# Optimization experiments

Measured on AMD Instinct MI355X. Metric: run time of the kernel, lower is better.

## Reference

```python
import jax, jax.numpy as jnp
import numpy as np

B, H, W, D = 16, 14, 14, 512   # map_dim D == attention_dim A (required by broadcast add)
L, HID, A = 32, 512, 512


def setup_inputs() -> dict:
    key = jax.random.key(0)
    ks = jax.random.split(key, 8)
    s = 0.02
    return {
        "maps": jax.random.normal(ks[0], (B, H, W, D), jnp.float32),
        "hiddens": jax.random.normal(ks[1], (B, L, HID), jnp.float32),
        "W_hidden": jax.random.normal(ks[2], (A, HID), jnp.float32) * s,
        "b_hidden": jnp.zeros((A,), jnp.float32),
        "W_rect": jax.random.normal(ks[3], (1, A), jnp.float32) * s,
        "b_rect": jnp.zeros((1,), jnp.float32),
        "W_co": jax.random.normal(ks[4], (HID, D), jnp.float32) * s,
        "b_co": jnp.zeros((HID,), jnp.float32),
    }


def reference(maps, hiddens, W_hidden, b_hidden, W_rect, b_rect, W_co, b_co):
    b, h, w, d = maps.shape
    fmaps = maps.reshape(b, h * w, d)                       # (B, P, D)
    hlin = hiddens @ W_hidden.T + b_hidden                  # (B, L, A)
    # additive co-attention score: ReLU(fmaps + hlin) -> linear to scalar
    rect = jax.nn.relu(fmaps[:, None, :, :] + hlin[:, :, None, :])  # (B, L, P, A)
    scores = jnp.einsum('blpa,a->blp', rect, W_rect[0]) + b_rect[0]  # (B, L, P)
    attn = jax.nn.softmax(scores, axis=2)                   # softmax over pixels P
    ctx = jnp.einsum('blp,bpd->bld', attn, fmaps)           # (B, L, D)
    co_att = (ctx @ W_co.T + b_co) * hiddens                # (B, L, HID)
    return co_att, attn
```

## Files before the change

### kernel.cpp

```cpp
#include <hip/hip_runtime.h>
#include <math.h>


typedef __attribute__((ext_vector_type(8))) short short8;
typedef __attribute__((ext_vector_type(4))) float f32x4;

__device__ __forceinline__ unsigned f2bf_u(float x) {
    union { float f; unsigned u; } c; c.f = x;
    return (c.u + 0x7FFFu + ((c.u >> 16) & 1u)) >> 16;
}
__device__ __forceinline__ unsigned pack2(float lo, float hi) {
    return f2bf_u(lo) | (f2bf_u(hi) << 16);
}
__device__ __forceinline__ uint4 pack8(const float4 a, const float4 b) {
    uint4 r;
    r.x = pack2(a.x, a.y); r.y = pack2(a.z, a.w);
    r.z = pack2(b.x, b.y); r.w = pack2(b.z, b.w);
    return r;
}
__device__ __forceinline__ float rdot4(const float4 f, const float4 g, const float4 w) {
    return fmaxf(f.x+g.x, 0.f)*w.x + fmaxf(f.y+g.y, 0.f)*w.y
         + fmaxf(f.z+g.z, 0.f)*w.z + fmaxf(f.w+g.w, 0.f)*w.w;
}
__device__ __forceinline__ float wave_sum(float v) {
    v += __shfl_down(v, 32); v += __shfl_down(v, 16); v += __shfl_down(v, 8);
    v += __shfl_down(v, 4);  v += __shfl_down(v, 2);  v += __shfl_down(v, 1);
    return v;
}

template<int HMUL>
__global__ __launch_bounds__(512) void gemm_kernel(
    const float* __restrict__ Af, const float* __restrict__ Bf,
    const float* __restrict__ bias, const float* __restrict__ hmul,
    float* __restrict__ C)
{
    __shared__ __align__(16) char smem[65536];
    uint4* As = (uint4*)smem;
    uint4* Bs = (uint4*)(smem + 32768);
    float* red = (float*)smem;
    const int tid = threadIdx.x, bid = blockIdx.x;

    const int m0 = (bid >> 4) * 32, n0 = (bid & 15) * 32;
    #pragma unroll
    for (int j = 0; j < 4; ++j) {
        const int S = tid + 512 * j;
        const int i = S >> 6, ln = S & 63;
        const int t = i & 1, s = i >> 1;
        const int row  = t * 16 + (ln & 15);
        const int col8 = s * 4 + (ln >> 4);
        const float* ap = Af + (size_t)(m0 + row) * 512 + col8 * 8;
        const float* bp = Bf + (size_t)(n0 + row) * 512 + col8 * 8;
        As[S] = pack8(*(const float4*)ap, *(const float4*)(ap + 4));
        Bs[S] = pack8(*(const float4*)bp, *(const float4*)(bp + 4));
    }
    __syncthreads();

    const int w = tid >> 6, ln = tid & 63;
    f32x4 acc[4];
    #pragma unroll
    for (int fo = 0; fo < 4; ++fo) acc[fo] = (f32x4){0.f,0.f,0.f,0.f};
    #pragma unroll
    for (int sl = 0; sl < 2; ++sl) {
        const int s = 2 * w + sl;
        const short8 a0 = *(const short8*)&As[(2*s+0)*64 + ln];
        const short8 a1 = *(const short8*)&As[(2*s+1)*64 + ln];
        const short8 b0 = *(const short8*)&Bs[(2*s+0)*64 + ln];
        const short8 b1 = *(const short8*)&Bs[(2*s+1)*64 + ln];
        acc[0] = __builtin_amdgcn_mfma_f32_16x16x32_bf16(a0, b0, acc[0], 0, 0, 0);
        acc[1] = __builtin_amdgcn_mfma_f32_16x16x32_bf16(a0, b1, acc[1], 0, 0, 0);
        acc[2] = __builtin_amdgcn_mfma_f32_16x16x32_bf16(a1, b0, acc[2], 0, 0, 0);
        acc[3] = __builtin_amdgcn_mfma_f32_16x16x32_bf16(a1, b1, acc[3], 0, 0, 0);
    }
    __syncthreads();
    #pragma unroll
    for (int fo = 0; fo < 4; ++fo)
        #pragma unroll
        for (int r = 0; r < 4; ++r)
            red[w*1024 + fo*256 + r*64 + ln] = acc[fo][r];
    __syncthreads();
    #pragma unroll
    for (int jj = 0; jj < 2; ++jj) {
        const int o = tid + 512 * jj;
        float v = 0.f;
        #pragma unroll
        for (int ww = 0; ww < 8; ++ww) v += red[ww*1024 + o];
        const int fo = o >> 8, r = (o >> 6) & 3, l2 = o & 63;
        const int m = m0 + (fo >> 1) * 16 + ((l2 >> 4) << 2) + r;
        const int n = n0 + (fo & 1) * 16 + (l2 & 15);
        v += bias[n];
        if (HMUL) v *= hmul[(size_t)m * 512 + n];
        C[(size_t)m * 512 + n] = v;
    }
}

__global__ __launch_bounds__(512) void mid_kernel(
    const float* __restrict__ maps, const float* __restrict__ hlin,
    const float* __restrict__ W_rect, const float* __restrict__ b_rect,
    float* __restrict__ attn_out, float* __restrict__ ctx_out)
{
    __shared__ float smrow[2 * 208];
    const int tid = threadIdx.x, bx = blockIdx.x;
    const int xcd = bx & 7, idx = bx >> 3;
    const int b  = (xcd << 1) | (idx & 1);
    const int l0 = (idx >> 1) * 2;
    const int w = tid >> 6, lane = tid & 63;
    const int a_lo = lane * 4, a_hi = 256 + lane * 4;

    const float* h0p = hlin + ((size_t)b * 32 + l0) * 512;
    const float* h1p = h0p + 512;
    const float4 g0_lo = *(const float4*)(h0p + a_lo);
    const float4 g0_hi = *(const float4*)(h0p + a_hi);
    const float4 g1_lo = *(const float4*)(h1p + a_lo);
    const float4 g1_hi = *(const float4*)(h1p + a_hi);
    const float4 w_lo  = *(const float4*)(W_rect + a_lo);
    const float4 w_hi  = *(const float4*)(W_rect + a_hi);
    const float br = b_rect[0];
    const float* mb = maps + (size_t)b * 196 * 512;

    for (int p0 = w; p0 < 196; p0 += 8) {
        const float* fr = mb + (size_t)p0 * 512;
        const float4 fa = *(const float4*)(fr + a_lo);
        const float4 fb = *(const float4*)(fr + a_hi);
        float sA = rdot4(fa, g0_lo, w_lo) + rdot4(fb, g0_hi, w_hi);
        float sB = rdot4(fa, g1_lo, w_lo) + rdot4(fb, g1_hi, w_hi);
        sA = wave_sum(sA);
        sB = wave_sum(sB);
        if (lane == 0) { smrow[p0] = sA + br; smrow[208 + p0] = sB + br; }
    }
    __syncthreads();

    if (w < 2) {
        float v[4];
        #pragma unroll
        for (int i = 0; i < 4; ++i) {
            const int p = lane + 64 * i;
            v[i] = (p < 196) ? smrow[w * 208 + p] : -INFINITY;
        }
        float m = fmaxf(fmaxf(v[0], v[1]), fmaxf(v[2], v[3]));
        for (int off = 32; off > 0; off >>= 1) m = fmaxf(m, __shfl_down(m, off));
        m = __shfl(m, 0);
        float e[4], ssum = 0.f;
        #pragma unroll
        for (int i = 0; i < 4; ++i) {
            const int p = lane + 64 * i;
            e[i] = (p < 196) ? __expf(v[i] - m) : 0.f;
            ssum += e[i];
        }
        for (int off = 32; off > 0; off >>= 1) ssum += __shfl_down(ssum, off);
        ssum = __shfl(ssum, 0);
        const float inv = 1.f / ssum;
        float* ao = attn_out + ((size_t)b * 32 + l0 + w) * 196;
        #pragma unroll
        for (int i = 0; i < 4; ++i) {
            const int p = lane + 64 * i;
            if (p < 196) {
                const float at = e[i] * inv;
                smrow[w * 208 + p] = at;
                ao[p] = at;
            }
        }
    }
    __syncthreads();

    {
        const int d = tid;
        float a0=0.f,a1=0.f,a2=0.f,a3=0.f, c0=0.f,c1=0.f,c2=0.f,c3=0.f;
        for (int p = 0; p < 196; p += 4) {
            const float f0 = mb[(size_t)(p+0)*512 + d];
            const float f1 = mb[(size_t)(p+1)*512 + d];
            const float f2 = mb[(size_t)(p+2)*512 + d];
            const float f3 = mb[(size_t)(p+3)*512 + d];
            a0 += smrow[p+0]*f0; a1 += smrow[p+1]*f1;
            a2 += smrow[p+2]*f2; a3 += smrow[p+3]*f3;
            c0 += smrow[208+p+0]*f0; c1 += smrow[208+p+1]*f1;
            c2 += smrow[208+p+2]*f2; c3 += smrow[208+p+3]*f3;
        }
        float* cx = ctx_out + ((size_t)b * 32 + l0) * 512;
        cx[d]       = (a0 + a1) + (a2 + a3);
        cx[512 + d] = (c0 + c1) + (c2 + c3);
    }
}

extern "C" void kernel_launch(void* const* d_in, const int* in_sizes, int n_in,
                              void* d_out, int out_size, void* d_ws, size_t ws_size,
                              hipStream_t stream)
{
    const float* maps     = (const float*)d_in[0];
    const float* hiddens  = (const float*)d_in[1];
    const float* W_hidden = (const float*)d_in[2];
    const float* b_hidden = (const float*)d_in[3];
    const float* W_rect   = (const float*)d_in[4];
    const float* b_rect   = (const float*)d_in[5];
    const float* W_co     = (const float*)d_in[6];
    const float* b_co     = (const float*)d_in[7];

    float* out_co   = (float*)d_out;
    float* out_attn = out_co + (size_t)512 * 512;
    float* hlin     = (float*)d_ws;
    float* ctx      = hlin + (size_t)512 * 512;

    hipLaunchKernelGGL((gemm_kernel<0>), dim3(256), dim3(512), 0, stream,
                       hiddens, W_hidden, b_hidden, (const float*)nullptr, hlin);
    hipLaunchKernelGGL(mid_kernel, dim3(256), dim3(512), 0, stream,
                       maps, hlin, W_rect, b_rect, out_attn, ctx);
    hipLaunchKernelGGL((gemm_kernel<1>), dim3(256), dim3(512), 0, stream,
                       ctx, W_co, b_co, hiddens, out_co);
}
```

Before: 105.9 us.

## Fuse three kernels into one persistent kernel with per-batch flag synchronization

Merges the hidden-projection GEMM, the attention/softmax/context stage and the output GEMM into a single launch of 256 blocks. Blocks signal per-batch completion through global atomic counters and spin-wait on the batch they depend on, with an epoch counter so repeated calls reuse the flags. The aim is to remove two kernel launch boundaries and their drain/fill gaps. The cost is relaxed atomic loads and stores for the intermediate buffers. It also depends on all 256 blocks being co-resident, and a capped spin could fall through before data is ready.

```diff
diff --git a/kernel.cpp b/kernel.cpp
--- a/kernel.cpp
+++ b/kernel.cpp
@@ -4,6 +4,28 @@
 
 typedef __attribute__((ext_vector_type(8))) short short8;
 typedef __attribute__((ext_vector_type(4))) float f32x4;
+
+__device__ unsigned g_flag1[16];
+__device__ unsigned g_flag2[16];
+__device__ unsigned g_blk[256];
+
+#define SPIN_CAP 200000u
+
+__device__ __forceinline__ float2 cload2(const float* p) {
+    unsigned long long v = __hip_atomic_load((const unsigned long long*)p,
+                                             __ATOMIC_RELAXED, __HIP_MEMORY_SCOPE_AGENT);
+    union { unsigned long long u; float2 f; } c; c.u = v;
+    return c.f;
+}
+__device__ __forceinline__ void cstore(float* p, float v) {
+    __hip_atomic_store(p, v, __ATOMIC_RELAXED, __HIP_MEMORY_SCOPE_AGENT);
+}
+__device__ __forceinline__ unsigned frelax(unsigned* p) {
+    return __hip_atomic_fetch_add(p, 1u, __ATOMIC_RELAXED, __HIP_MEMORY_SCOPE_AGENT);
+}
+__device__ __forceinline__ unsigned lrelax(const unsigned* p) {
+    return __hip_atomic_load(p, __ATOMIC_RELAXED, __HIP_MEMORY_SCOPE_AGENT);
+}
 
 __device__ __forceinline__ unsigned f2bf_u(float x) {
     union { float f; unsigned u; } c; c.f = x;
@@ -28,13 +50,12 @@
     return v;
 }
 
-template<int HMUL>
-__global__ __launch_bounds__(512) void gemm_kernel(
+template<int HMUL, int CLOADA, int CSTOREC>
+__device__ __forceinline__ void gemm_body(char* smem,
     const float* __restrict__ Af, const float* __restrict__ Bf,
     const float* __restrict__ bias, const float* __restrict__ hmul,
     float* __restrict__ C)
 {
-    __shared__ __align__(16) char smem[65536];
     uint4* As = (uint4*)smem;
     uint4* Bs = (uint4*)(smem + 32768);
     float* red = (float*)smem;
@@ -50,7 +71,16 @@
         const int col8 = s * 4 + (ln >> 4);
         const float* ap = Af + (size_t)(m0 + row) * 512 + col8 * 8;
         const float* bp = Bf + (size_t)(n0 + row) * 512 + col8 * 8;
-        As[S] = pack8(*(const float4*)ap, *(const float4*)(ap + 4));
+        float4 av0, av1;
+        if (CLOADA) {
+            const float2 p0 = cload2(ap + 0), p1 = cload2(ap + 2);
+            const float2 p2 = cload2(ap + 4), p3 = cload2(ap + 6);
+            av0.x = p0.x; av0.y = p0.y; av0.z = p1.x; av0.w = p1.y;
+            av1.x = p2.x; av1.y = p2.y; av1.z = p3.x; av1.w = p3.y;
+        } else {
+            av0 = *(const float4*)ap; av1 = *(const float4*)(ap + 4);
+        }
+        As[S] = pack8(av0, av1);
         Bs[S] = pack8(*(const float4*)bp, *(const float4*)(bp + 4));
     }
     __syncthreads();
@@ -89,29 +119,31 @@
         const int n = n0 + (fo & 1) * 16 + (l2 & 15);
         v += bias[n];
         if (HMUL) v *= hmul[(size_t)m * 512 + n];
-        C[(size_t)m * 512 + n] = v;
-    }
-}
-
-__global__ __launch_bounds__(512) void mid_kernel(
+        if (CSTOREC) cstore(&C[(size_t)m * 512 + n], v);
+        else         C[(size_t)m * 512 + n] = v;
+    }
+}
+
+__device__ __forceinline__ void mid_body(float* smrow, int b, int l0,
     const float* __restrict__ maps, const float* __restrict__ hlin,
     const float* __restrict__ W_rect, const float* __restrict__ b_rect,
     float* __restrict__ attn_out, float* __restrict__ ctx_out)
 {
-    __shared__ float smrow[2 * 208];
-    const int tid = threadIdx.x, bx = blockIdx.x;
-    const int xcd = bx & 7, idx = bx >> 3;
-    const int b  = (xcd << 1) | (idx & 1);
-    const int l0 = (idx >> 1) * 2;
+    const int tid = threadIdx.x;
     const int w = tid >> 6, lane = tid & 63;
     const int a_lo = lane * 4, a_hi = 256 + lane * 4;
 
     const float* h0p = hlin + ((size_t)b * 32 + l0) * 512;
     const float* h1p = h0p + 512;
-    const float4 g0_lo = *(const float4*)(h0p + a_lo);
-    const float4 g0_hi = *(const float4*)(h0p + a_hi);
-    const float4 g1_lo = *(const float4*)(h1p + a_lo);
-    const float4 g1_hi = *(const float4*)(h1p + a_hi);
+    float4 g0_lo, g0_hi, g1_lo, g1_hi;
+    { const float2 x = cload2(h0p+a_lo), y = cload2(h0p+a_lo+2);
+      g0_lo.x = x.x; g0_lo.y = x.y; g0_lo.z = y.x; g0_lo.w = y.y; }
+    { const float2 x = cload2(h0p+a_hi), y = cload2(h0p+a_hi+2);
+      g0_hi.x = x.x; g0_hi.y = x.y; g0_hi.z = y.x; g0_hi.w = y.y; }
+    { const float2 x = cload2(h1p+a_lo), y = cload2(h1p+a_lo+2);
+      g1_lo.x = x.x; g1_lo.y = x.y; g1_lo.z = y.x; g1_lo.w = y.y; }
+    { const float2 x = cload2(h1p+a_hi), y = cload2(h1p+a_hi+2);
+      g1_hi.x = x.x; g1_hi.y = x.y; g1_hi.z = y.x; g1_hi.w = y.y; }
     const float4 w_lo  = *(const float4*)(W_rect + a_lo);
     const float4 w_hi  = *(const float4*)(W_rect + a_hi);
     const float br = b_rect[0];
@@ -176,9 +208,55 @@
             c2 += smrow[208+p+2]*f2; c3 += smrow[208+p+3]*f3;
         }
         float* cx = ctx_out + ((size_t)b * 32 + l0) * 512;
-        cx[d]       = (a0 + a1) + (a2 + a3);
-        cx[512 + d] = (c0 + c1) + (c2 + c3);
-    }
+        cstore(cx + d,       (a0 + a1) + (a2 + a3));
+        cstore(cx + 512 + d, (c0 + c1) + (c2 + c3));
+    }
+}
+
+__global__ __launch_bounds__(512) void coatt_flow(
+    const float* __restrict__ maps, const float* __restrict__ hiddens,
+    const float* __restrict__ W_hidden, const float* __restrict__ b_hidden,
+    const float* __restrict__ W_rect, const float* __restrict__ b_rect,
+    const float* __restrict__ W_co, const float* __restrict__ b_co,
+    float* __restrict__ out_co, float* __restrict__ attn_out,
+    float* __restrict__ hlin_ws, float* __restrict__ ctx_ws)
+{
+    __shared__ __align__(16) char smem[65536];
+    __shared__ __align__(16) float smrow[2 * 208];
+    __shared__ unsigned s_r;
+
+    const int tid = threadIdx.x, bx = blockIdx.x;
+    const int b_gemm = bx >> 4;
+    const int b_mid  = ((bx & 7) << 1) | ((bx >> 3) & 1);
+    const int l0     = (bx >> 4) * 2;
+
+    if (tid == 0)
+        s_r = frelax(&g_blk[bx]);
+    __syncthreads();
+    const unsigned tgt = 16u * (s_r + 1u);
+
+    gemm_body<0, 0, 1>(smem, hiddens, W_hidden, b_hidden,
+                       (const float*)nullptr, hlin_ws);
+    __syncthreads();
+    if (tid == 0) {
+        frelax(&g_flag1[b_gemm]);
+        unsigned it = 0;
+        while (lrelax(&g_flag1[b_mid]) < tgt && ++it < SPIN_CAP)
+            __builtin_amdgcn_s_sleep(8);
+    }
+    __syncthreads();
+
+    mid_body(smrow, b_mid, l0, maps, hlin_ws, W_rect, b_rect, attn_out, ctx_ws);
+    __syncthreads();
+    if (tid == 0) {
+        frelax(&g_flag2[b_mid]);
+        unsigned it = 0;
+        while (lrelax(&g_flag2[b_gemm]) < tgt && ++it < SPIN_CAP)
+            __builtin_amdgcn_s_sleep(8);
+    }
+    __syncthreads();
+
+    gemm_body<1, 1, 0>(smem, ctx_ws, W_co, b_co, hiddens, out_co);
 }
 
 extern "C" void kernel_launch(void* const* d_in, const int* in_sizes, int n_in,
@@ -199,10 +277,7 @@
     float* hlin     = (float*)d_ws;
     float* ctx      = hlin + (size_t)512 * 512;
 
-    hipLaunchKernelGGL((gemm_kernel<0>), dim3(256), dim3(512), 0, stream,
-                       hiddens, W_hidden, b_hidden, (const float*)nullptr, hlin);
-    hipLaunchKernelGGL(mid_kernel, dim3(256), dim3(512), 0, stream,
-                       maps, hlin, W_rect, b_rect, out_attn, ctx);
-    hipLaunchKernelGGL((gemm_kernel<1>), dim3(256), dim3(512), 0, stream,
-                       ctx, W_co, b_co, hiddens, out_co);
-}
+    hipLaunchKernelGGL(coatt_flow, dim3(256), dim3(512), 0, stream,
+                       maps, hiddens, W_hidden, b_hidden, W_rect, b_rect,
+                       W_co, b_co, out_co, out_attn, hlin, ctx);
+}
```

Result: slower. 117.8 us (+11.2%).
